# Optimization experiments

Measured on AMD Instinct MI355X. Metric: run time of the kernel, lower is better.

## Reference

```python
import jax, jax.numpy as jnp
import numpy as np

B, S, H, I, E_ROUTED, TOP_K = 8, 2048, 1024, 2048, 8, 2


def _expert(x, Wg, Wu, Wd):
    # SwiGLU expert: down(silu(gate(x)) * up(x)); Linear weights stored [out, in]
    return (jax.nn.silu(x @ Wg.T) * (x @ Wu.T)) @ Wd.T


def setup_inputs() -> dict:
    key = jax.random.key(0)
    ks = jax.random.split(key, 9)
    s = 0.02  # init scale
    return {
        "x": jax.random.normal(ks[0], (B, S, H), dtype=jnp.float32),
        # shared expert (num_shared = 1)
        "Wg_s": jax.random.normal(ks[1], (I, H), dtype=jnp.float32) * s,
        "Wu_s": jax.random.normal(ks[2], (I, H), dtype=jnp.float32) * s,
        "Wd_s": jax.random.normal(ks[3], (H, I), dtype=jnp.float32) * s,
        # routed experts, stacked [E, ...]
        "Wg": jax.random.normal(ks[4], (E_ROUTED, I, H), dtype=jnp.float32) * s,
        "Wu": jax.random.normal(ks[5], (E_ROUTED, I, H), dtype=jnp.float32) * s,
        "Wd": jax.random.normal(ks[6], (E_ROUTED, H, I), dtype=jnp.float32) * s,
        # router
        "Wr": jax.random.normal(ks[7], (E_ROUTED, H), dtype=jnp.float32) * s,
        "rb": jnp.zeros((E_ROUTED,), dtype=jnp.float32),
    }


def reference(x, Wg_s, Wu_s, Wd_s, Wg, Wu, Wd, Wr, rb):
    # shared experts (num_shared = 1, so mean == the single expert output)
    shared = _expert(x, Wg_s, Wu_s, Wd_s)  # [B,S,H]

    # sigmoid top-k routing
    logits = jnp.einsum('bsh,eh->bse', x, Wr) + rb        # [B,S,E]
    probs = jax.nn.sigmoid(logits)
    scores, idx = jax.lax.top_k(probs, TOP_K)             # [B,S,K]

    # dense combine weights: cw[b,s,e] = sum_k scores[b,s,k] * 1[idx[b,s,k]==e]
    cw = (jax.nn.one_hot(idx, E_ROUTED, dtype=x.dtype) * scores[..., None]).sum(-2)  # [B,S,E]

    out = shared
    for e in range(E_ROUTED):  # small fixed expert count
        out = out + cw[..., e:e + 1] * _expert(x, Wg[e], Wu[e], Wd[e])
    return out
```

## Files before the change

kernel.cpp:

```cpp
#include <hip/hip_runtime.h>

#define T_TOK 16384
#define HDIM  1024
#define IDIM  2048
#define NEXP  8
#define CNT_STRIDE 32
#define TOK_PER_BLK 32
#define MAX_TILES 400

typedef __attribute__((ext_vector_type(8))) short bf16x8;
typedef __attribute__((ext_vector_type(4))) float f32x4;
typedef unsigned short u16;
typedef unsigned int u32;

typedef __attribute__((address_space(1))) const unsigned int gas_u32;
typedef __attribute__((address_space(3))) unsigned int las_u32;

__device__ __forceinline__ void gl16(const void* g, void* l) {
  __builtin_amdgcn_global_load_lds((gas_u32*)g, (las_u32*)l, 16, 0, 0);
}

__device__ __forceinline__ u16 f2bf(float f) {
  union { float f; u32 i; } v; v.f = f;
  u32 r = v.i + 0x7FFF + ((v.i >> 16) & 1);
  return (u16)(r >> 16);
}
__device__ __forceinline__ u32 pack2(float a, float b) {
  return (u32)f2bf(a) | ((u32)f2bf(b) << 16);
}

__global__ __launch_bounds__(256) void cvt_kernel(
    const float* __restrict__ s, u16* __restrict__ d, int n)
{
  int i = (blockIdx.x * 256 + threadIdx.x) * 4;
  if (i < n) {
    f32x4 v = *(const f32x4*)(s + i);
    uint2 o; o.x = pack2(v[0], v[1]); o.y = pack2(v[2], v[3]);
    *(uint2*)(d + i) = o;
  }
}

__global__ void init_counts(int* counts) {
  counts[threadIdx.x] = 0;
}

__global__ __launch_bounds__(256) void zero_kernel(float* __restrict__ p, int n4) {
  f32x4 z = {0.f, 0.f, 0.f, 0.f};
  for (int i = blockIdx.x * 256 + threadIdx.x; i < n4; i += gridDim.x * 256)
    ((f32x4*)p)[i] = z;
}

__global__ __launch_bounds__(256) void router_kernel(
    const float* __restrict__ x, const float* __restrict__ Wr,
    const float* __restrict__ rb, float* __restrict__ cw,
    int* __restrict__ counts, int* __restrict__ lists)
{
  __shared__ __align__(16) float sWr[NEXP * HDIM];
  __shared__ int pickE[2 * TOK_PER_BLK];
  __shared__ int pickT[2 * TOK_PER_BLK];

  const int tid = threadIdx.x;
  const int lane = tid & 63;
  const int wv = tid >> 6;

  for (int i = tid; i < NEXP * HDIM / 4; i += 256)
    ((f32x4*)sWr)[i] = ((const f32x4*)Wr)[i];

  float rbl[NEXP];
  #pragma unroll
  for (int e = 0; e < NEXP; ++e) rbl[e] = rb[e];

  __syncthreads();

  const int t_base = blockIdx.x * TOK_PER_BLK + wv * (TOK_PER_BLK / 4);
  for (int j = 0; j < TOK_PER_BLK / 4; ++j) {
    const int t = t_base + j;
    const float* xrow = x + (size_t)t * HDIM;
    f32x4 xv[4];
    #pragma unroll
    for (int c = 0; c < 4; ++c) xv[c] = *(const f32x4*)(xrow + c * 256 + lane * 4);

    double acc[NEXP];
    #pragma unroll
    for (int e = 0; e < NEXP; ++e) {
      const float* wr = sWr + e * HDIM;
      double a = 0.0;
      #pragma unroll
      for (int c = 0; c < 4; ++c) {
        f32x4 w4 = *(const f32x4*)(wr + c * 256 + lane * 4);
        a += (double)xv[c][0] * (double)w4[0];
        a += (double)xv[c][1] * (double)w4[1];
        a += (double)xv[c][2] * (double)w4[2];
        a += (double)xv[c][3] * (double)w4[3];
      }
      acc[e] = a;
    }
    #pragma unroll
    for (int e = 0; e < NEXP; ++e) {
      double a = acc[e];
      a += __shfl_xor(a, 1, 64);
      a += __shfl_xor(a, 2, 64);
      a += __shfl_xor(a, 4, 64);
      acc[e] = a;
    }
    double s0 = (lane & 1) ? acc[1] : acc[0];
    double s1 = (lane & 1) ? acc[3] : acc[2];
    double s2 = (lane & 1) ? acc[5] : acc[4];
    double s3 = (lane & 1) ? acc[7] : acc[6];
    double u0 = (lane & 2) ? s1 : s0;
    double u1 = (lane & 2) ? s3 : s2;
    double v  = (lane & 4) ? u1 : u0;
    v += __shfl_xor(v, 8, 64);
    v += __shfl_xor(v, 16, 64);
    v += __shfl_xor(v, 32, 64);
    double l[NEXP];
    #pragma unroll
    for (int e = 0; e < NEXP; ++e) l[e] = __shfl(v, e, 64) + (double)rbl[e];

    if (lane == 0) {
      int i1 = 0;
      #pragma unroll
      for (int e = 1; e < NEXP; ++e) if (l[e] > l[i1]) i1 = e;
      int i2 = -1;
      #pragma unroll
      for (int e = 0; e < NEXP; ++e) {
        if (e == i1) continue;
        if (i2 < 0 || l[e] > l[i2]) i2 = e;
      }
      float p1 = (float)(1.0 / (1.0 + exp(-l[i1])));
      float p2 = (float)(1.0 / (1.0 + exp(-l[i2])));
      cw[(size_t)t * NEXP + i1] = p1;
      cw[(size_t)t * NEXP + i2] = p2;
      int slot = (wv * (TOK_PER_BLK / 4) + j) * 2;
      pickE[slot] = i1; pickE[slot + 1] = i2;
      pickT[slot] = t;  pickT[slot + 1] = t;
    }
  }
  __syncthreads();

  const int myE = pickE[lane];
  const int myT = pickT[lane];
  #pragma unroll
  for (int ei = 0; ei < 2; ++ei) {
    int e = wv + ei * 4;
    unsigned long long b = __ballot(myE == e);
    int cnt = __popcll(b);
    int base = 0;
    if (lane == 0) base = atomicAdd(&counts[e * CNT_STRIDE], cnt);
    base = __shfl(base, 0, 64);
    if (myE == e)
      lists[(size_t)e * T_TOK + base + __popcll(b & ((1ull << lane) - 1))] = myT;
  }
}

__global__ void build_tiles(const int* __restrict__ counts,
                            int* __restrict__ td_e, int* __restrict__ td_r0,
                            int* __restrict__ ntiles)
{
  if (threadIdx.x == 0) {
    int n = 0;
    for (int r = 0; r < T_TOK; r += 128) { td_e[n] = -1; td_r0[n] = r; ++n; }
    for (int e = 0; e < NEXP; ++e) {
      int c = counts[e * CNT_STRIDE];
      for (int r = 0; r < c; r += 128) { td_e[n] = e; td_r0[n] = r; ++n; }
    }
    *ntiles = n;
  }
}


__global__ __launch_bounds__(256, 2) void gateup128f(
    const u16* __restrict__ xb,
    const u16* __restrict__ Wg_sh, const u16* __restrict__ Wu_sh,
    const u16* __restrict__ Wg_rt, const u16* __restrict__ Wu_rt,
    const int* __restrict__ lists, const int* __restrict__ counts,
    const int* __restrict__ td_e, const int* __restrict__ td_r0,
    const int* __restrict__ ntiles,
    u16* __restrict__ hbuf, int t0)
{
  __shared__ __align__(16) u16 sA[128 * 64];
  __shared__ __align__(16) u16 sG[128 * 64];
  __shared__ __align__(16) u16 sU[128 * 64];

  const int ty = t0 + blockIdx.y;
  if (ty >= *ntiles) return;
  const int e = td_e[ty];
  const int r0 = td_r0[ty];
  const size_t WSH = (size_t)IDIM * HDIM;
  int cnt; const int* list; const u16 *Wg_e, *Wu_e;
  if (e < 0) { cnt = T_TOK; list = nullptr; Wg_e = Wg_sh; Wu_e = Wu_sh; }
  else {
    cnt = counts[e * CNT_STRIDE]; list = lists + (size_t)e * T_TOK;
    Wg_e = Wg_rt + (size_t)e * WSH; Wu_e = Wu_rt + (size_t)e * WSH;
  }
  const int n0 = blockIdx.x * 128;

  const int tid = threadIdx.x, lane = tid & 63, w = tid >> 6;
  const int wm = w & 1, wn = w >> 1;
  const int quad = lane >> 4, l15 = lane & 15, l7 = lane & 7;
  const int drow = lane >> 3;
  const int sslot = (lane & 7) ^ drow;

  const u16 *pa[4], *pg[4], *pu[4];
  u16 *dA[4], *dG[4], *dU[4];
  #pragma unroll
  for (int c = 0; c < 4; ++c) {
    int row = w * 32 + c * 8 + drow;
    int gi = r0 + row;
    int tok = list ? ((gi < cnt) ? list[gi] : 0) : gi;
    pa[c] = xb + (size_t)tok * HDIM + sslot * 8;
    pg[c] = Wg_e + (size_t)(n0 + row) * HDIM + sslot * 8;
    pu[c] = Wu_e + (size_t)(n0 + row) * HDIM + sslot * 8;
    dA[c] = sA + (w * 32 + c * 8) * 64;
    dG[c] = sG + (w * 32 + c * 8) * 64;
    dU[c] = sU + (w * 32 + c * 8) * 64;
  }

  const u16* fA = sA + (wm * 64 + l15) * 64;
  const u16* fG = sG + (wn * 64 + l15) * 64;
  const u16* fU = sU + (wn * 64 + l15) * 64;

  f32x4 accG[4][4] = {};
  f32x4 accU[4][4] = {};

  for (int kt = 0; kt < HDIM / 64; ++kt) {
    #pragma unroll
    for (int c = 0; c < 4; ++c) {
      gl16(pa[c] + kt * 64, dA[c]);
      gl16(pg[c] + kt * 64, dG[c]);
      gl16(pu[c] + kt * 64, dU[c]);
    }
    __syncthreads();
    #pragma unroll
    for (int ks = 0; ks < 2; ++ks) {
      const int sw = ((ks * 4 + quad) ^ l7) * 8;
      bf16x8 a[4], bg[4], bu[4];
      #pragma unroll
      for (int mt = 0; mt < 4; ++mt) a[mt] = *(const bf16x8*)(fA + mt * 1024 + sw);
      #pragma unroll
      for (int nt = 0; nt < 4; ++nt) {
        bg[nt] = *(const bf16x8*)(fG + nt * 1024 + sw);
        bu[nt] = *(const bf16x8*)(fU + nt * 1024 + sw);
      }
      #pragma unroll
      for (int nt = 0; nt < 4; ++nt) {
        #pragma unroll
        for (int mt = 0; mt < 4; ++mt) {
          accG[mt][nt] = __builtin_amdgcn_mfma_f32_16x16x32_bf16(a[mt], bg[nt], accG[mt][nt], 0, 0, 0);
          accU[mt][nt] = __builtin_amdgcn_mfma_f32_16x16x32_bf16(a[mt], bu[nt], accU[mt][nt], 0, 0, 0);
        }
      }
    }
    __syncthreads();
  }

  #pragma unroll
  for (int mt = 0; mt < 4; ++mt) {
    #pragma unroll
    for (int i = 0; i < 4; ++i) {
      int rl = wm * 64 + mt * 16 + quad * 4 + i;
      u16* orow = hbuf + (size_t)(blockIdx.y * 128 + rl) * IDIM + n0 + wn * 64 + l15;
      #pragma unroll
      for (int nt = 0; nt < 4; ++nt) {
        float g = accG[mt][nt][i], u = accU[mt][nt][i];
        float h = (g / (1.f + __expf(-g))) * u;
        orow[nt * 16] = f2bf(h);
      }
    }
  }
}

__global__ __launch_bounds__(256, 2) void down256f(
    const u16* __restrict__ hbuf,
    const u16* __restrict__ Wd_sh, const u16* __restrict__ Wd_rt,
    const int* __restrict__ lists, const int* __restrict__ counts,
    const int* __restrict__ td_e, const int* __restrict__ td_r0,
    const int* __restrict__ ntiles,
    const float* __restrict__ cw, float* __restrict__ out, int t0)
{
  __shared__ __align__(16) u16 sA[128 * 64];
  __shared__ __align__(16) u16 sB[256 * 64];

  const int ty = t0 + blockIdx.y;
  if (ty >= *ntiles) return;
  const int e = td_e[ty];
  const int r0 = td_r0[ty];
  const size_t WSH = (size_t)IDIM * HDIM;
  int cnt; const int* list; const u16* Wd_e;
  if (e < 0) { cnt = T_TOK; list = nullptr; Wd_e = Wd_sh; }
  else {
    cnt = counts[e * CNT_STRIDE]; list = lists + (size_t)e * T_TOK;
    Wd_e = Wd_rt + (size_t)e * WSH;
  }
  const int n0 = blockIdx.x * 256;

  const int tid = threadIdx.x, lane = tid & 63, w = tid >> 6;
  const int wm = w & 1, wn = w >> 1;
  const int quad = lane >> 4, l15 = lane & 15, l7 = lane & 7;
  const int drow = lane >> 3;
  const int sslot = (lane & 7) ^ drow;

  const u16 *pa[4], *pb[8];
  u16 *dA[4], *dB[8];
  #pragma unroll
  for (int c = 0; c < 4; ++c) {
    int row = w * 32 + c * 8 + drow;
    pa[c] = hbuf + (size_t)(blockIdx.y * 128 + row) * IDIM + sslot * 8;
    dA[c] = sA + (w * 32 + c * 8) * 64;
  }
  #pragma unroll
  for (int c = 0; c < 8; ++c) {
    int row = w * 64 + c * 8 + drow;
    pb[c] = Wd_e + (size_t)(n0 + row) * IDIM + sslot * 8;
    dB[c] = sB + (w * 64 + c * 8) * 64;
  }

  const u16* fA = sA + (wm * 64 + l15) * 64;
  const u16* fB = sB + (wn * 128 + l15) * 64;

  f32x4 acc[4][8] = {};

  for (int kt = 0; kt < IDIM / 64; ++kt) {
    #pragma unroll
    for (int c = 0; c < 4; ++c) gl16(pa[c] + kt * 64, dA[c]);
    #pragma unroll
    for (int c = 0; c < 8; ++c) gl16(pb[c] + kt * 64, dB[c]);
    __syncthreads();
    #pragma unroll
    for (int ks = 0; ks < 2; ++ks) {
      const int sw = ((ks * 4 + quad) ^ l7) * 8;
      bf16x8 a[4], b[8];
      #pragma unroll
      for (int mt = 0; mt < 4; ++mt) a[mt] = *(const bf16x8*)(fA + mt * 1024 + sw);
      #pragma unroll
      for (int nt = 0; nt < 8; ++nt) b[nt] = *(const bf16x8*)(fB + nt * 1024 + sw);
      #pragma unroll
      for (int nt = 0; nt < 8; ++nt) {
        #pragma unroll
        for (int mt = 0; mt < 4; ++mt)
          acc[mt][nt] = __builtin_amdgcn_mfma_f32_16x16x32_bf16(a[mt], b[nt], acc[mt][nt], 0, 0, 0);
      }
    }
    __syncthreads();
  }

  #pragma unroll
  for (int mt = 0; mt < 4; ++mt) {
    #pragma unroll
    for (int i = 0; i < 4; ++i) {
      int rl = wm * 64 + mt * 16 + quad * 4 + i;
      if (r0 + rl < cnt) {
        int token = list ? list[r0 + rl] : (r0 + rl);
        float s = (e >= 0) ? cw[(size_t)token * NEXP + e] : 1.f;
        float* orow = out + (size_t)token * HDIM + n0 + wn * 128 + l15;
        #pragma unroll
        for (int nt = 0; nt < 8; ++nt)
          atomicAdd(&orow[nt * 16], s * acc[mt][nt][i]);
      }
    }
  }
}

__global__ __launch_bounds__(256, 2) void moe_gateup_k(
    const float* __restrict__ xf,
    const float* __restrict__ Wg_f, const float* __restrict__ Wu_f,
    const int* __restrict__ list, const int* __restrict__ count_ptr,
    u16* __restrict__ hbuf, int c0)
{
  __shared__ __align__(16) u16 sA[128 * 32];
  __shared__ __align__(16) u16 sG[128 * 32];
  __shared__ __align__(16) u16 sU[128 * 32];

  const int cnt = count_ptr ? *count_ptr : T_TOK;
  const int remain = cnt - c0;
  const int m0 = blockIdx.y * 128;
  if (m0 >= remain) return;
  const int n0 = blockIdx.x * 128;

  const int tid = threadIdx.x, lane = tid & 63, w = tid >> 6;
  const int wm = w & 1, wn = w >> 1;
  const int quad = lane >> 4, l15 = lane & 15;
  const int ar = lane >> 3, ac = lane & 7;

  const float *fa[4], *fg[4], *fu[4];
  int frow[4];
  #pragma unroll
  for (int p = 0; p < 4; ++p) {
    int row = w * 32 + p * 8 + ar;
    frow[p] = row;
    int gi = c0 + m0 + row;
    int tok = (gi < cnt) ? (list ? list[gi] : gi) : 0;
    fa[p] = xf + (size_t)tok * HDIM + ac * 4;
    fg[p] = Wg_f + (size_t)(n0 + row) * HDIM + ac * 4;
    fu[p] = Wu_f + (size_t)(n0 + row) * HDIM + ac * 4;
  }

  const u16* fA = sA + (wm * 64 + l15) * 32 + quad * 8;
  const u16* fG = sG + (wn * 64 + l15) * 32 + quad * 8;
  const u16* fU = sU + (wn * 64 + l15) * 32 + quad * 8;

  f32x4 accG[4][4] = {};
  f32x4 accU[4][4] = {};

  for (int kt = 0; kt < HDIM / 32; ++kt) {
    #pragma unroll
    for (int p = 0; p < 4; ++p) {
      f32x4 va = *(const f32x4*)(fa[p] + kt * 32);
      f32x4 vg = *(const f32x4*)(fg[p] + kt * 32);
      f32x4 vu = *(const f32x4*)(fu[p] + kt * 32);
      uint2 oa; oa.x = pack2(va[0], va[1]); oa.y = pack2(va[2], va[3]);
      uint2 og; og.x = pack2(vg[0], vg[1]); og.y = pack2(vg[2], vg[3]);
      uint2 ou; ou.x = pack2(vu[0], vu[1]); ou.y = pack2(vu[2], vu[3]);
      *(uint2*)(sA + frow[p] * 32 + ac * 4) = oa;
      *(uint2*)(sG + frow[p] * 32 + ac * 4) = og;
      *(uint2*)(sU + frow[p] * 32 + ac * 4) = ou;
    }
    __syncthreads();
    bf16x8 a[4];
    #pragma unroll
    for (int mt = 0; mt < 4; ++mt) a[mt] = *(const bf16x8*)(fA + mt * 16 * 32);
    #pragma unroll
    for (int nt = 0; nt < 4; ++nt) {
      bf16x8 bg = *(const bf16x8*)(fG + nt * 16 * 32);
      bf16x8 bu = *(const bf16x8*)(fU + nt * 16 * 32);
      #pragma unroll
      for (int mt = 0; mt < 4; ++mt) {
        accG[mt][nt] = __builtin_amdgcn_mfma_f32_16x16x32_bf16(a[mt], bg, accG[mt][nt], 0, 0, 0);
        accU[mt][nt] = __builtin_amdgcn_mfma_f32_16x16x32_bf16(a[mt], bu, accU[mt][nt], 0, 0, 0);
      }
    }
    __syncthreads();
  }

  #pragma unroll
  for (int mt = 0; mt < 4; ++mt) {
    #pragma unroll
    for (int i = 0; i < 4; ++i) {
      int row = m0 + wm * 64 + mt * 16 + quad * 4 + i;
      if (row < remain) {
        u16* orow = hbuf + (size_t)row * IDIM + n0 + wn * 64 + l15;
        #pragma unroll
        for (int nt = 0; nt < 4; ++nt) {
          float g = accG[mt][nt][i], u = accU[mt][nt][i];
          float h = (g / (1.f + __expf(-g))) * u;
          orow[nt * 16] = f2bf(h);
        }
      }
    }
  }
}

__global__ __launch_bounds__(256, 2) void moe_down_k(
    const u16* __restrict__ hbuf, const float* __restrict__ Wd_f,
    const int* __restrict__ list, const int* __restrict__ count_ptr,
    const float* __restrict__ cw, int expert, float* __restrict__ out, int c0)
{
  __shared__ __align__(16) u16 sA[128 * 32];
  __shared__ __align__(16) u16 sB[128 * 32];

  const int cnt = count_ptr ? *count_ptr : T_TOK;
  const int remain = cnt - c0;
  const int m0 = blockIdx.y * 128;
  if (m0 >= remain) return;
  const int n0 = blockIdx.x * 128;

  const int tid = threadIdx.x, lane = tid & 63, w = tid >> 6;
  const int wm = w & 1, wn = w >> 1;
  const int quad = lane >> 4, l15 = lane & 15;

  const int srow0 = w * 32 + (lane >> 2);
  const int srow1 = srow0 + 16;
  const int kch = (lane & 3) * 8;
  const int ar = lane >> 3, ac = lane & 7;

  const u16* pa0 = hbuf + (size_t)(m0 + srow0) * IDIM + kch;
  const u16* pa1 = hbuf + (size_t)(m0 + srow1) * IDIM + kch;
  const float* fb[4];
  int frow[4];
  #pragma unroll
  for (int p = 0; p < 4; ++p) {
    int row = w * 32 + p * 8 + ar;
    frow[p] = row;
    fb[p] = Wd_f + (size_t)(n0 + row) * IDIM + ac * 4;
  }

  const u16* fA = sA + (wm * 64 + l15) * 32 + quad * 8;
  const u16* fB = sB + (wn * 64 + l15) * 32 + quad * 8;

  f32x4 acc[4][4] = {};

  for (int kt = 0; kt < IDIM / 32; ++kt) {
    gl16(pa0 + kt * 32, sA + w * 1024);
    gl16(pa1 + kt * 32, sA + w * 1024 + 512);
    #pragma unroll
    for (int p = 0; p < 4; ++p) {
      f32x4 v = *(const f32x4*)(fb[p] + kt * 32);
      uint2 o; o.x = pack2(v[0], v[1]); o.y = pack2(v[2], v[3]);
      *(uint2*)(sB + frow[p] * 32 + ac * 4) = o;
    }
    __syncthreads();
    bf16x8 a[4];
    #pragma unroll
    for (int mt = 0; mt < 4; ++mt) a[mt] = *(const bf16x8*)(fA + mt * 16 * 32);
    #pragma unroll
    for (int nt = 0; nt < 4; ++nt) {
      bf16x8 b = *(const bf16x8*)(fB + nt * 16 * 32);
      #pragma unroll
      for (int mt = 0; mt < 4; ++mt)
        acc[mt][nt] = __builtin_amdgcn_mfma_f32_16x16x32_bf16(a[mt], b, acc[mt][nt], 0, 0, 0);
    }
    __syncthreads();
  }

  #pragma unroll
  for (int mt = 0; mt < 4; ++mt) {
    #pragma unroll
    for (int i = 0; i < 4; ++i) {
      int rl = m0 + wm * 64 + mt * 16 + quad * 4 + i;
      if (rl < remain) {
        int token = list ? list[c0 + rl] : (c0 + rl);
        float s = (expert >= 0) ? cw[(size_t)token * NEXP + expert] : 1.f;
        float* orow = out + (size_t)token * HDIM + n0 + wn * 64 + l15;
        #pragma unroll
        for (int nt = 0; nt < 4; ++nt) {
          float v = s * acc[mt][nt][i];
          if (expert >= 0) v += orow[nt * 16];
          orow[nt * 16] = v;
        }
      }
    }
  }
}

extern "C" void kernel_launch(void* const* d_in, const int* in_sizes, int n_in,
                              void* d_out, int out_size, void* d_ws, size_t ws_size,
                              hipStream_t stream) {
  (void)in_sizes; (void)n_in; (void)out_size;
  const float* x    = (const float*)d_in[0];
  const float* Wg_s = (const float*)d_in[1];
  const float* Wu_s = (const float*)d_in[2];
  const float* Wd_s = (const float*)d_in[3];
  const float* Wg   = (const float*)d_in[4];
  const float* Wu   = (const float*)d_in[5];
  const float* Wd   = (const float*)d_in[6];
  const float* Wr   = (const float*)d_in[7];
  const float* rb   = (const float*)d_in[8];
  float* out = (float*)d_out;

  char* ws = (char*)d_ws;
  size_t off = 1024;
  int* counts = (int*)ws;
  int* lists = (int*)(ws + off);  off += (size_t)NEXP * T_TOK * 4;
  float* cw = (float*)(ws + off); off += (size_t)T_TOK * NEXP * 4;
  int* td = (int*)(ws + off);     off += 3328;
  int* td_e = td;
  int* td_r0 = td + MAX_TILES;
  int* ntiles = td + 2 * MAX_TILES;

  const size_t WSH = (size_t)IDIM * HDIM;
  const size_t xc_elems = (size_t)T_TOK * HDIM;
  const size_t wc_elems = 3 * WSH + 3 * NEXP * WSH;
  const size_t fast_need = off + (xc_elems + wc_elems) * 2 + (size_t)2048 * IDIM * 2;
  const bool fast = ws_size >= fast_need;

  u16* xc = (u16*)(ws + off);
  u16* wgs_c = xc + (fast ? xc_elems : 0);
  u16* wus_c = wgs_c + WSH;
  u16* wds_c = wus_c + WSH;
  u16* wg_c = wds_c + WSH;
  u16* wu_c = wg_c + NEXP * WSH;
  u16* wd_c = wu_c + NEXP * WSH;

  size_t hoff = off + (fast ? (xc_elems + wc_elems) * 2 : 0);
  u16* hbuf = (u16*)(ws + hoff);

  size_t avail = (ws_size > hoff) ? (ws_size - hoff) : 0;
  long long capll = (long long)(avail / ((size_t)IDIM * 2));
  int cap = (capll > (long long)MAX_TILES * 128) ? MAX_TILES * 128 : (int)capll;
  cap &= ~127;
  if (cap < 128) cap = 128;

  init_counts<<<1, NEXP * CNT_STRIDE, 0, stream>>>(counts);
  if (fast) {
    zero_kernel<<<2048, 256, 0, stream>>>(out, (int)(xc_elems / 4));
    auto cv = [&](const float* s, u16* d, size_t n) {
      int blocks = (int)((n / 4 + 255) / 256);
      cvt_kernel<<<blocks, 256, 0, stream>>>(s, d, (int)n);
    };
    cv(x, xc, xc_elems);
    cv(Wg_s, wgs_c, WSH); cv(Wu_s, wus_c, WSH); cv(Wd_s, wds_c, WSH);
    cv(Wg, wg_c, NEXP * WSH); cv(Wu, wu_c, NEXP * WSH); cv(Wd, wd_c, NEXP * WSH);
  }
  router_kernel<<<T_TOK / TOK_PER_BLK, 256, 0, stream>>>(x, Wr, rb, cw, counts, lists);

  if (fast) {
    build_tiles<<<1, 64, 0, stream>>>(counts, td_e, td_r0, ntiles);
    int tpc = cap / 128;
    for (int t0 = 0; t0 < MAX_TILES; t0 += tpc) {
      int yt = (MAX_TILES - t0 < tpc) ? (MAX_TILES - t0) : tpc;
      gateup128f<<<dim3(IDIM / 128, yt), 256, 0, stream>>>(
          xc, wgs_c, wus_c, wg_c, wu_c, lists, counts, td_e, td_r0, ntiles, hbuf, t0);
      down256f<<<dim3(HDIM / 256, yt), 256, 0, stream>>>(
          hbuf, wds_c, wd_c, lists, counts, td_e, td_r0, ntiles, cw, out, t0);
    }
  } else {
    int fcap = cap;
    int nchunks = (T_TOK + fcap - 1) / fcap;
    dim3 blk(256);
    dim3 gA(IDIM / 128, fcap / 128);
    dim3 gB(HDIM / 128, fcap / 128);
    for (int c = 0; c < nchunks; ++c) {
      int c0 = c * fcap;
      moe_gateup_k<<<gA, blk, 0, stream>>>(x, Wg_s, Wu_s, nullptr, nullptr, hbuf, c0);
      moe_down_k<<<gB, blk, 0, stream>>>(hbuf, Wd_s, nullptr, nullptr, cw, -1, out, c0);
    }
    for (int e = 0; e < NEXP; ++e) {
      const int* lst = lists + (size_t)e * T_TOK;
      const int* cptr = counts + (size_t)e * CNT_STRIDE;
      for (int c = 0; c < nchunks; ++c) {
        int c0 = c * fcap;
        moe_gateup_k<<<gA, blk, 0, stream>>>(x, Wg + (size_t)e * WSH, Wu + (size_t)e * WSH,
                                             lst, cptr, hbuf, c0);
        moe_down_k<<<gB, blk, 0, stream>>>(hbuf, Wd + (size_t)e * WSH,
                                           lst, cptr, cw, e, out, c0);
      }
    }
  }
}
```

Before: 1.216 ms.

## Split shared-expert pass with plain stores, drop output zeroing, batch weight conversions

Runs the shared expert as a separate first pass whose down-projection writes the output with plain stores instead of atomics. This removes the zero-fill kernel and the atomic traffic for the shared contribution. Routed tiles then accumulate with atomics in later passes, with chunking capped at 132 tiles per launch. Weight conversions are merged into two three-way launches, and the router now runs before the conversions. The routed tile table shrinks to 264 entries, which assumes the routed tile count never exceeds that bound.

Measured after the change: 1.156 ms. 1.05x faster.

```diff
diff --git a/kernel.cpp b/kernel.cpp
--- a/kernel.cpp
+++ b/kernel.cpp
@@ -6,7 +6,8 @@
 #define NEXP  8
 #define CNT_STRIDE 32
 #define TOK_PER_BLK 32
-#define MAX_TILES 400
+#define MAX_RT 264
+#define SH_TILES (T_TOK / 128)
 
 typedef __attribute__((ext_vector_type(8))) short bf16x8;
 typedef __attribute__((ext_vector_type(4))) float f32x4;
@@ -40,14 +41,23 @@
   }
 }
 
+__global__ __launch_bounds__(256) void cvt3_kernel(
+    const float* __restrict__ s0, const float* __restrict__ s1,
+    const float* __restrict__ s2,
+    u16* __restrict__ d0, u16* __restrict__ d1, u16* __restrict__ d2, int n)
+{
+  const float* s = (blockIdx.z == 0) ? s0 : (blockIdx.z == 1) ? s1 : s2;
+  u16* d = (blockIdx.z == 0) ? d0 : (blockIdx.z == 1) ? d1 : d2;
+  int i = (blockIdx.x * 256 + threadIdx.x) * 4;
+  if (i < n) {
+    f32x4 v = *(const f32x4*)(s + i);
+    uint2 o; o.x = pack2(v[0], v[1]); o.y = pack2(v[2], v[3]);
+    *(uint2*)(d + i) = o;
+  }
+}
+
 __global__ void init_counts(int* counts) {
   counts[threadIdx.x] = 0;
-}
-
-__global__ __launch_bounds__(256) void zero_kernel(float* __restrict__ p, int n4) {
-  f32x4 z = {0.f, 0.f, 0.f, 0.f};
-  for (int i = blockIdx.x * 256 + threadIdx.x; i < n4; i += gridDim.x * 256)
-    ((f32x4*)p)[i] = z;
 }
 
 __global__ __launch_bounds__(256) void router_kernel(
@@ -159,7 +169,6 @@
 {
   if (threadIdx.x == 0) {
     int n = 0;
-    for (int r = 0; r < T_TOK; r += 128) { td_e[n] = -1; td_r0[n] = r; ++n; }
     for (int e = 0; e < NEXP; ++e) {
       int c = counts[e * CNT_STRIDE];
       for (int r = 0; r < c; r += 128) { td_e[n] = e; td_r0[n] = r; ++n; }
@@ -176,22 +185,23 @@
     const int* __restrict__ lists, const int* __restrict__ counts,
     const int* __restrict__ td_e, const int* __restrict__ td_r0,
     const int* __restrict__ ntiles,
-    u16* __restrict__ hbuf, int t0)
+    u16* __restrict__ hbuf, int t0, int routed)
 {
   __shared__ __align__(16) u16 sA[128 * 64];
   __shared__ __align__(16) u16 sG[128 * 64];
   __shared__ __align__(16) u16 sU[128 * 64];
 
-  const int ty = t0 + blockIdx.y;
-  if (ty >= *ntiles) return;
-  const int e = td_e[ty];
-  const int r0 = td_r0[ty];
   const size_t WSH = (size_t)IDIM * HDIM;
-  int cnt; const int* list; const u16 *Wg_e, *Wu_e;
-  if (e < 0) { cnt = T_TOK; list = nullptr; Wg_e = Wg_sh; Wu_e = Wu_sh; }
-  else {
-    cnt = counts[e * CNT_STRIDE]; list = lists + (size_t)e * T_TOK;
+  int r0, cnt; const int* list; const u16 *Wg_e, *Wu_e;
+  if (routed) {
+    int ty = t0 + blockIdx.y;
+    if (ty >= *ntiles) return;
+    int e = td_e[ty]; r0 = td_r0[ty]; cnt = counts[e * CNT_STRIDE];
+    list = lists + (size_t)e * T_TOK;
     Wg_e = Wg_rt + (size_t)e * WSH; Wu_e = Wu_rt + (size_t)e * WSH;
+  } else {
+    r0 = (t0 + blockIdx.y) * 128; cnt = T_TOK; list = nullptr;
+    Wg_e = Wg_sh; Wu_e = Wu_sh;
   }
   const int n0 = blockIdx.x * 128;
 
@@ -276,21 +286,22 @@
     const int* __restrict__ lists, const int* __restrict__ counts,
     const int* __restrict__ td_e, const int* __restrict__ td_r0,
     const int* __restrict__ ntiles,
-    const float* __restrict__ cw, float* __restrict__ out, int t0)
+    const float* __restrict__ cw, float* __restrict__ out, int t0, int routed)
 {
   __shared__ __align__(16) u16 sA[128 * 64];
   __shared__ __align__(16) u16 sB[256 * 64];
 
-  const int ty = t0 + blockIdx.y;
-  if (ty >= *ntiles) return;
-  const int e = td_e[ty];
-  const int r0 = td_r0[ty];
   const size_t WSH = (size_t)IDIM * HDIM;
-  int cnt; const int* list; const u16* Wd_e;
-  if (e < 0) { cnt = T_TOK; list = nullptr; Wd_e = Wd_sh; }
-  else {
-    cnt = counts[e * CNT_STRIDE]; list = lists + (size_t)e * T_TOK;
+  int e = -1, r0, cnt; const int* list; const u16* Wd_e;
+  if (routed) {
+    int ty = t0 + blockIdx.y;
+    if (ty >= *ntiles) return;
+    e = td_e[ty]; r0 = td_r0[ty]; cnt = counts[e * CNT_STRIDE];
+    list = lists + (size_t)e * T_TOK;
     Wd_e = Wd_rt + (size_t)e * WSH;
+  } else {
+    r0 = (t0 + blockIdx.y) * 128; cnt = T_TOK; list = nullptr;
+    Wd_e = Wd_sh;
   }
   const int n0 = blockIdx.x * 256;
 
@@ -350,12 +361,19 @@
     for (int i = 0; i < 4; ++i) {
       int rl = wm * 64 + mt * 16 + quad * 4 + i;
       if (r0 + rl < cnt) {
-        int token = list ? list[r0 + rl] : (r0 + rl);
-        float s = (e >= 0) ? cw[(size_t)token * NEXP + e] : 1.f;
-        float* orow = out + (size_t)token * HDIM + n0 + wn * 128 + l15;
-        #pragma unroll
-        for (int nt = 0; nt < 8; ++nt)
-          atomicAdd(&orow[nt * 16], s * acc[mt][nt][i]);
+        if (routed) {
+          int token = list[r0 + rl];
+          float s = cw[(size_t)token * NEXP + e];
+          float* orow = out + (size_t)token * HDIM + n0 + wn * 128 + l15;
+          #pragma unroll
+          for (int nt = 0; nt < 8; ++nt)
+            atomicAdd(&orow[nt * 16], s * acc[mt][nt][i]);
+        } else {
+          float* orow = out + (size_t)(r0 + rl) * HDIM + n0 + wn * 128 + l15;
+          #pragma unroll
+          for (int nt = 0; nt < 8; ++nt)
+            orow[nt * 16] = acc[mt][nt][i];
+        }
       }
     }
   }
@@ -552,10 +570,10 @@
   int* counts = (int*)ws;
   int* lists = (int*)(ws + off);  off += (size_t)NEXP * T_TOK * 4;
   float* cw = (float*)(ws + off); off += (size_t)T_TOK * NEXP * 4;
-  int* td = (int*)(ws + off);     off += 3328;
+  int* td = (int*)(ws + off);     off += 2304;
   int* td_e = td;
-  int* td_r0 = td + MAX_TILES;
-  int* ntiles = td + 2 * MAX_TILES;
+  int* td_r0 = td + MAX_RT;
+  int* ntiles = td + 2 * MAX_RT;
 
   const size_t WSH = (size_t)IDIM * HDIM;
   const size_t xc_elems = (size_t)T_TOK * HDIM;
@@ -575,36 +593,45 @@
   u16* hbuf = (u16*)(ws + hoff);
 
   size_t avail = (ws_size > hoff) ? (ws_size - hoff) : 0;
-  long long capll = (long long)(avail / ((size_t)IDIM * 2));
-  int cap = (capll > (long long)MAX_TILES * 128) ? MAX_TILES * 128 : (int)capll;
-  cap &= ~127;
-  if (cap < 128) cap = 128;
+  long long ct = (long long)(avail / ((size_t)128 * IDIM * 2));
+  int cap_tiles = (ct > MAX_RT) ? MAX_RT : (int)ct;
+  if (cap_tiles < 1) cap_tiles = 1;
+  int tpc = (cap_tiles < 132) ? cap_tiles : 132;
 
   init_counts<<<1, NEXP * CNT_STRIDE, 0, stream>>>(counts);
+  router_kernel<<<T_TOK / TOK_PER_BLK, 256, 0, stream>>>(x, Wr, rb, cw, counts, lists);
+
   if (fast) {
-    zero_kernel<<<2048, 256, 0, stream>>>(out, (int)(xc_elems / 4));
-    auto cv = [&](const float* s, u16* d, size_t n) {
-      int blocks = (int)((n / 4 + 255) / 256);
-      cvt_kernel<<<blocks, 256, 0, stream>>>(s, d, (int)n);
-    };
-    cv(x, xc, xc_elems);
-    cv(Wg_s, wgs_c, WSH); cv(Wu_s, wus_c, WSH); cv(Wd_s, wds_c, WSH);
-    cv(Wg, wg_c, NEXP * WSH); cv(Wu, wu_c, NEXP * WSH); cv(Wd, wd_c, NEXP * WSH);
-  }
-  router_kernel<<<T_TOK / TOK_PER_BLK, 256, 0, stream>>>(x, Wr, rb, cw, counts, lists);
-
-  if (fast) {
+    {
+      int n = (int)xc_elems;
+      cvt_kernel<<<(n / 4 + 255) / 256, 256, 0, stream>>>(x, xc, n);
+      int ns = (int)WSH;
+      dim3 gs((ns / 4 + 255) / 256, 1, 3);
+      cvt3_kernel<<<gs, 256, 0, stream>>>(Wg_s, Wu_s, Wd_s, wgs_c, wus_c, wds_c, ns);
+      int nr = (int)(NEXP * WSH);
+      dim3 gr((nr / 4 + 255) / 256, 1, 3);
+      cvt3_kernel<<<gr, 256, 0, stream>>>(Wg, Wu, Wd, wg_c, wu_c, wd_c, nr);
+    }
     build_tiles<<<1, 64, 0, stream>>>(counts, td_e, td_r0, ntiles);
-    int tpc = cap / 128;
-    for (int t0 = 0; t0 < MAX_TILES; t0 += tpc) {
-      int yt = (MAX_TILES - t0 < tpc) ? (MAX_TILES - t0) : tpc;
+
+    for (int t0 = 0; t0 < SH_TILES; t0 += tpc) {
+      int yt = (SH_TILES - t0 < tpc) ? (SH_TILES - t0) : tpc;
       gateup128f<<<dim3(IDIM / 128, yt), 256, 0, stream>>>(
-          xc, wgs_c, wus_c, wg_c, wu_c, lists, counts, td_e, td_r0, ntiles, hbuf, t0);
+          xc, wgs_c, wus_c, wg_c, wu_c, lists, counts, td_e, td_r0, ntiles,
+          hbuf, t0, 0);
       down256f<<<dim3(HDIM / 256, yt), 256, 0, stream>>>(
-          hbuf, wds_c, wd_c, lists, counts, td_e, td_r0, ntiles, cw, out, t0);
+          hbuf, wds_c, wd_c, lists, counts, td_e, td_r0, ntiles, cw, out, t0, 0);
+    }
+    for (int t0 = 0; t0 < MAX_RT; t0 += tpc) {
+      int yt = (MAX_RT - t0 < tpc) ? (MAX_RT - t0) : tpc;
+      gateup128f<<<dim3(IDIM / 128, yt), 256, 0, stream>>>(
+          xc, wgs_c, wus_c, wg_c, wu_c, lists, counts, td_e, td_r0, ntiles,
+          hbuf, t0, 1);
+      down256f<<<dim3(HDIM / 256, yt), 256, 0, stream>>>(
+          hbuf, wds_c, wd_c, lists, counts, td_e, td_r0, ntiles, cw, out, t0, 1);
     }
   } else {
-    int fcap = cap;
+    int fcap = tpc * 128;
     int nchunks = (T_TOK + fcap - 1) / fcap;
     dim3 blk(256);
     dim3 gA(IDIM / 128, fcap / 128);
```
